# Kernel tuning notes

Hardware: AMD Instinct MI355X
Metric: run time of the kernel (lower is better)

The kernel has to match this reference:

```python
import jax, jax.numpy as jnp
import numpy as np

B, K, Z = 16384, 4096, 64  # batch, codebook size, code dim


def _linear_params(key, fan_in, fan_out):
    kw, kb = jax.random.split(key)
    lim = 1.0 / np.sqrt(fan_in)
    W = jax.random.uniform(kw, (fan_out, fan_in), jnp.float32, -lim, lim)
    b = jax.random.uniform(kb, (fan_out,), jnp.float32, -lim, lim)
    return W, b


def setup_inputs() -> dict:
    key = jax.random.key(0)
    ks = jax.random.split(key, 10)
    X = jax.random.normal(ks[0], (B, 784), jnp.float32)
    We1, be1 = _linear_params(ks[1], 784, 1000)
    We2, be2 = _linear_params(ks[2], 1000, 500)
    We3, be3 = _linear_params(ks[3], 500, 300)
    We4, be4 = _linear_params(ks[4], 300, Z)
    emb = jax.random.normal(ks[5], (K, Z), jnp.float32)  # nn.Embedding default N(0,1)
    Wd1, bd1 = _linear_params(ks[6], Z, 300)
    Wd2, bd2 = _linear_params(ks[7], 300, 500)
    Wd3, bd3 = _linear_params(ks[8], 500, 1000)
    Wd4, bd4 = _linear_params(ks[9], 1000, 784)
    return dict(X=X, We1=We1, be1=be1, We2=We2, be2=be2, We3=We3, be3=be3,
                We4=We4, be4=be4, emb=emb, Wd1=Wd1, bd1=bd1, Wd2=Wd2, bd2=bd2,
                Wd3=Wd3, bd3=bd3, Wd4=Wd4, bd4=bd4)


def _lin(x, W, b):
    return x @ W.T + b


def _nearest(query, target):
    # squared euclidean distances [Q, T] via expanded form (same math, no QxTxZ blowup)
    q2 = jnp.sum(query * query, axis=1, keepdims=True)        # [Q,1]
    t2 = jnp.sum(target * target, axis=1)                      # [T]
    d = q2 - 2.0 * (query @ target.T) + t2[None, :]            # [Q,T]
    idx = jnp.argmin(d, axis=1)                                # first min, like torch .min
    return target[idx]


def reference(X, We1, be1, We2, be2, We3, be3, We4, be4, emb,
              Wd1, bd1, Wd2, bd2, Wd3, bd3, Wd4, bd4):
    x = X.reshape(-1, 784)
    h = jax.nn.relu(_lin(x, We1, be1))
    h = jax.nn.relu(_lin(h, We2, be2))
    h = jax.nn.relu(_lin(h, We3, be3))
    Z_enc = _lin(h, We4, be4)                                  # [B,Z]
    Z_emb = _nearest(Z_enc, emb)                               # [B,Z]
    d = jax.nn.leaky_relu(_lin(Z_emb, Wd1, bd1), 0.1)
    d = jax.nn.leaky_relu(_lin(d, Wd2, bd2), 0.1)
    d = jax.nn.leaky_relu(_lin(d, Wd3, bd3), 0.1)
    Z_dec = jnp.tanh(_lin(d, Wd4, bd4)).reshape(-1, 1, 28, 28)
    Z_enc_for_emb = _nearest(emb, Z_enc)                       # [K,Z]
    return (Z_dec, Z_enc, Z_dec, Z_enc_for_emb)
```

## Files before the change

### kernel.cpp

```cpp
#include <hip/hip_runtime.h>
#include <hip/hip_bf16.h>
#include <math.h>

typedef __bf16 bf16_t;
typedef __bf16 bf16x8 __attribute__((ext_vector_type(8)));
typedef __bf16 bf16x4 __attribute__((ext_vector_type(4)));
typedef float f32x4 __attribute__((ext_vector_type(4)));

__device__ __forceinline__ void gload16(const void* g, void* l)
{
    __builtin_amdgcn_global_load_lds(
        (const __attribute__((address_space(1))) void*)g,
        (__attribute__((address_space(3))) void*)l, 16, 0, 0);
}

template<int ACT, int RB>
__global__ __launch_bounds__(256)
void np_gemm(const float* __restrict__ A, const float* __restrict__ W,
             const float* __restrict__ bias, float* __restrict__ C,
             int N, int K)
{
    constexpr int LDA = RB * 64 + 4;
    constexpr int LDB = 128 + 4;
    __shared__ __align__(16) float sA[16][LDA];
    __shared__ __align__(16) float sB[16][LDB];
    const int tid  = threadIdx.x;
    const int tx   = tid & 15, ty = tid >> 4;
    const int bRow = blockIdx.y * (RB * 64), bCol = blockIdx.x * 128;

    float4 acc[RB][2][4];
#pragma unroll
    for (int ib = 0; ib < RB; ++ib)
#pragma unroll
        for (int jb = 0; jb < 2; ++jb)
#pragma unroll
            for (int i = 0; i < 4; ++i)
                acc[ib][jb][i] = make_float4(0.f, 0.f, 0.f, 0.f);

    for (int k0 = 0; k0 < K; k0 += 16) {
        __syncthreads();
#pragma unroll
        for (int i = 0; i < RB; ++i) {
            int c  = tid + i * 256;
            int r  = c >> 2;
            int kc = (c & 3) << 2;
            int gk = k0 + kc;
            float4 av = make_float4(0.f, 0.f, 0.f, 0.f);
            if (gk < K) av = *(const float4*)(A + (size_t)(bRow + r) * K + gk);
            sA[kc + 0][r] = av.x; sA[kc + 1][r] = av.y;
            sA[kc + 2][r] = av.z; sA[kc + 3][r] = av.w;
        }
#pragma unroll
        for (int i = 0; i < 2; ++i) {
            int c  = tid + i * 256;
            int r  = c >> 2;
            int kc = (c & 3) << 2;
            int gk = k0 + kc;
            int gr = bCol + r;
            float4 bv = make_float4(0.f, 0.f, 0.f, 0.f);
            if (gr < N && gk < K) bv = *(const float4*)(W + (size_t)gr * K + gk);
            sB[kc + 0][r] = bv.x; sB[kc + 1][r] = bv.y;
            sB[kc + 2][r] = bv.z; sB[kc + 3][r] = bv.w;
        }
        __syncthreads();

#pragma unroll
        for (int kk = 0; kk < 16; ++kk) {
            float4 a[RB], b[2];
#pragma unroll
            for (int ib = 0; ib < RB; ++ib)
                a[ib] = *(const float4*)&sA[kk][ib * 64 + ty * 4];
            b[0] = *(const float4*)&sB[kk][tx * 4];
            b[1] = *(const float4*)&sB[kk][64 + tx * 4];
#pragma unroll
            for (int ib = 0; ib < RB; ++ib) {
                float ai[4] = {a[ib].x, a[ib].y, a[ib].z, a[ib].w};
#pragma unroll
                for (int i = 0; i < 4; ++i)
#pragma unroll
                    for (int jb = 0; jb < 2; ++jb) {
                        acc[ib][jb][i].x = __fmaf_rn(ai[i], b[jb].x, acc[ib][jb][i].x);
                        acc[ib][jb][i].y = __fmaf_rn(ai[i], b[jb].y, acc[ib][jb][i].y);
                        acc[ib][jb][i].z = __fmaf_rn(ai[i], b[jb].z, acc[ib][jb][i].z);
                        acc[ib][jb][i].w = __fmaf_rn(ai[i], b[jb].w, acc[ib][jb][i].w);
                    }
            }
        }
    }

#pragma unroll
    for (int jb = 0; jb < 2; ++jb) {
        int col = bCol + jb * 64 + tx * 4;
        if (col >= N) continue;
        float4 bb = *(const float4*)(bias + col);
#pragma unroll
        for (int ib = 0; ib < RB; ++ib)
#pragma unroll
            for (int i = 0; i < 4; ++i) {
                int row = bRow + ib * 64 + ty * 4 + i;
                float4 v = acc[ib][jb][i];
                float4 o;
                o.x = __fadd_rn(v.x, bb.x); o.y = __fadd_rn(v.y, bb.y);
                o.z = __fadd_rn(v.z, bb.z); o.w = __fadd_rn(v.w, bb.w);
                if (ACT == 1) {
                    o.x = o.x > 0.f ? o.x : 0.f; o.y = o.y > 0.f ? o.y : 0.f;
                    o.z = o.z > 0.f ? o.z : 0.f; o.w = o.w > 0.f ? o.w : 0.f;
                }
                *(float4*)(C + (size_t)row * N + col) = o;
            }
    }
}

__global__ void k_split(const float* __restrict__ src, bf16_t* __restrict__ hi,
                        bf16_t* __restrict__ lo, int rows, int K, int rowsP, int Kp)
{
    int e = blockIdx.x * 256 + threadIdx.x;
    if (e >= rowsP * Kp) return;
    int r = e / Kp, k = e - r * Kp;
    float v = (r < rows && k < K) ? src[(size_t)r * K + k] : 0.f;
    bf16_t h = (bf16_t)v;
    bf16_t l = (bf16_t)(v - (float)h);
    hi[e] = h; lo[e] = l;
}

template<int ACT, int OUT>
__global__ __launch_bounds__(256)
void gemm_planes(const bf16_t* __restrict__ Ahi, const bf16_t* __restrict__ Alo,
                 const bf16_t* __restrict__ Bhi, const bf16_t* __restrict__ Blo,
                 const float* __restrict__ bias,
                 float* __restrict__ C0, float* __restrict__ C1,
                 bf16_t* __restrict__ Phi, bf16_t* __restrict__ Plo,
                 int N, int Kp, int Kpn)
{
    __shared__ __align__(16) bf16_t sA[2][128][32];
    __shared__ __align__(16) bf16_t sB[2][128][32];

    const int tid  = threadIdx.x;
    const int bRow = blockIdx.y * 128;
    const int bCol = blockIdx.x * 128;
    const int wave = tid >> 6;
    const int lane = tid & 63;
    const int wr   = (wave >> 1) * 64;
    const int wc   = (wave & 1) * 64;
    const int quad = lane >> 4;
    const int l15  = lane & 15;

    f32x4 acc[4][4];
#pragma unroll
    for (int i = 0; i < 4; ++i)
#pragma unroll
        for (int j = 0; j < 4; ++j) acc[i][j] = (f32x4){0.f, 0.f, 0.f, 0.f};

    for (int k0 = 0; k0 < Kp; k0 += 32) {
        __syncthreads();
#pragma unroll
        for (int i = 0; i < 2; ++i) {
            int c    = tid + i * 256;
            int row  = c >> 2;
            int koff = (c & 3) << 3;
            size_t ga = (size_t)(bRow + row) * Kp + (k0 + koff);
            size_t gb = (size_t)(bCol + row) * Kp + (k0 + koff);
            gload16(Ahi + ga, &sA[0][row][koff]);
            gload16(Alo + ga, &sA[1][row][koff]);
            gload16(Bhi + gb, &sB[0][row][koff]);
            gload16(Blo + gb, &sB[1][row][koff]);
        }
        __syncthreads();

        bf16x8 af[2][4], bfr[2][4];
#pragma unroll
        for (int t = 0; t < 2; ++t)
#pragma unroll
            for (int i = 0; i < 4; ++i) {
                af[t][i]  = *(const bf16x8*)&sA[t][wr + i * 16 + l15][quad * 8];
                bfr[t][i] = *(const bf16x8*)&sB[t][wc + i * 16 + l15][quad * 8];
            }
#pragma unroll
        for (int i = 0; i < 4; ++i)
#pragma unroll
            for (int j = 0; j < 4; ++j)
#pragma unroll
                for (int ta = 0; ta < 2; ++ta)
#pragma unroll
                    for (int tb = 0; tb < 2 - ta; ++tb)
                        acc[i][j] = __builtin_amdgcn_mfma_f32_16x16x32_bf16(
                            af[ta][i], bfr[tb][j], acc[i][j], 0, 0, 0);
    }

#pragma unroll
    for (int j = 0; j < 4; ++j) {
        int col = bCol + wc + j * 16 + l15;
        if (OUT == 0) {
            if (col >= N) continue;
            float bv = bias[col];
#pragma unroll
            for (int i = 0; i < 4; ++i)
#pragma unroll
                for (int r = 0; r < 4; ++r) {
                    int row = bRow + wr + i * 16 + quad * 4 + r;
                    float v = acc[i][j][r] + bv;
                    if (ACT == 1)      v = v > 0.f ? v : 0.f;
                    else if (ACT == 2) v = v >= 0.f ? v : 0.1f * v;
                    else if (ACT == 3) v = tanhf(v);
                    size_t o = (size_t)row * N + col;
                    C0[o] = v;
                    if (C1) C1[o] = v;
                }
        } else {
            if (col >= Kpn) continue;
            const bool real = col < N;
            float bv = real ? bias[col] : 0.f;
#pragma unroll
            for (int i = 0; i < 4; ++i)
#pragma unroll
                for (int r = 0; r < 4; ++r) {
                    int row = bRow + wr + i * 16 + quad * 4 + r;
                    float v = 0.f;
                    if (real) {
                        v = acc[i][j][r] + bv;
                        if (ACT == 1)      v = v > 0.f ? v : 0.f;
                        else if (ACT == 2) v = v >= 0.f ? v : 0.1f * v;
                        else if (ACT == 3) v = tanhf(v);
                    }
                    bf16_t h = (bf16_t)v;
                    bf16_t l = (bf16_t)(v - (float)h);
                    size_t o = (size_t)row * Kpn + col;
                    Phi[o] = h; Plo[o] = l;
                }
        }
    }
}

__global__ __launch_bounds__(256)
void k_nearest(const float* __restrict__ Q, const float* __restrict__ C,
               const float* __restrict__ q2a, const float* __restrict__ cn2,
               int chunk, float* __restrict__ pd, int* __restrict__ pi)
{
    __shared__ __align__(16) float sc[64][64];
    __shared__ __align__(16) float sn[64];
    const int tid = threadIdx.x;
    const int q   = blockIdx.x * 256 + tid;
    const int G   = gridDim.y;

    float qr[64];
    const float4* qp = (const float4*)(Q + (size_t)q * 64);
#pragma unroll
    for (int i = 0; i < 16; ++i) ((float4*)qr)[i] = qp[i];
    const float q2 = q2a[q];

    float best = 3.4e38f;
    int   bi   = 0x7fffffff;
    const int c0 = blockIdx.y * chunk;

    for (int cb = 0; cb < chunk; cb += 64) {
        __syncthreads();
        const float4* gp = (const float4*)(C + (size_t)(c0 + cb) * 64);
#pragma unroll
        for (int i = 0; i < 4; ++i) {
            int e = tid + i * 256;
            ((float4*)&sc[0][0])[e] = gp[e];
        }
        if (tid < 64) sn[tid] = cn2[c0 + cb + tid];
        __syncthreads();

        for (int c = 0; c < 64; c += 4) {
            float a0 = 0.f, a1 = 0.f, a2 = 0.f, a3 = 0.f;
            const float4* e0 = (const float4*)&sc[c + 0][0];
            const float4* e1 = (const float4*)&sc[c + 1][0];
            const float4* e2p = (const float4*)&sc[c + 2][0];
            const float4* e3 = (const float4*)&sc[c + 3][0];
#pragma unroll
            for (int z = 0; z < 16; ++z) {
                float4 q4 = ((float4*)qr)[z];
                float4 v0 = e0[z], v1 = e1[z], v2 = e2p[z], v3 = e3[z];
                a0 = __fmaf_rn(q4.x, v0.x, a0); a0 = __fmaf_rn(q4.y, v0.y, a0);
                a0 = __fmaf_rn(q4.z, v0.z, a0); a0 = __fmaf_rn(q4.w, v0.w, a0);
                a1 = __fmaf_rn(q4.x, v1.x, a1); a1 = __fmaf_rn(q4.y, v1.y, a1);
                a1 = __fmaf_rn(q4.z, v1.z, a1); a1 = __fmaf_rn(q4.w, v1.w, a1);
                a2 = __fmaf_rn(q4.x, v2.x, a2); a2 = __fmaf_rn(q4.y, v2.y, a2);
                a2 = __fmaf_rn(q4.z, v2.z, a2); a2 = __fmaf_rn(q4.w, v2.w, a2);
                a3 = __fmaf_rn(q4.x, v3.x, a3); a3 = __fmaf_rn(q4.y, v3.y, a3);
                a3 = __fmaf_rn(q4.z, v3.z, a3); a3 = __fmaf_rn(q4.w, v3.w, a3);
            }
            float d;
            d = __fadd_rn(__fsub_rn(q2, __fmul_rn(2.f, a0)), sn[c + 0]);
            if (d < best) { best = d; bi = c0 + cb + c + 0; }
            d = __fadd_rn(__fsub_rn(q2, __fmul_rn(2.f, a1)), sn[c + 1]);
            if (d < best) { best = d; bi = c0 + cb + c + 1; }
            d = __fadd_rn(__fsub_rn(q2, __fmul_rn(2.f, a2)), sn[c + 2]);
            if (d < best) { best = d; bi = c0 + cb + c + 2; }
            d = __fadd_rn(__fsub_rn(q2, __fmul_rn(2.f, a3)), sn[c + 3]);
            if (d < best) { best = d; bi = c0 + cb + c + 3; }
        }
    }
    pd[(size_t)q * G + blockIdx.y] = best;
    pi[(size_t)q * G + blockIdx.y] = bi;
}

__global__ void k_reduce(const float* __restrict__ pd, const int* __restrict__ pi,
                         int G, int NQ, int* __restrict__ out)
{
    int q = blockIdx.x * blockDim.x + threadIdx.x;
    if (q >= NQ) return;
    float best = 3.4e38f; int bi = 0;
    for (int g = 0; g < G; ++g) {
        float d = pd[(size_t)q * G + g];
        if (d < best) { best = d; bi = pi[(size_t)q * G + g]; }
    }
    out[q] = bi;
}

__global__ void k_gather(const float* __restrict__ src, const int* __restrict__ idx,
                         float* __restrict__ dst, int nsrc)
{
    int r = blockIdx.x, z = threadIdx.x;
    int i = idx[r];
    i = i < 0 ? 0 : (i >= nsrc ? nsrc - 1 : i);
    dst[(size_t)r * 64 + z] = src[(size_t)i * 64 + z];
}

__global__ void k_gather_split(const float* __restrict__ src, const int* __restrict__ idx,
                               bf16_t* __restrict__ hi, bf16_t* __restrict__ lo, int nsrc)
{
    int r = blockIdx.x, z = threadIdx.x;
    int i = idx[r];
    i = i < 0 ? 0 : (i >= nsrc ? nsrc - 1 : i);
    float v = src[(size_t)i * 64 + z];
    bf16_t h = (bf16_t)v;
    bf16_t l = (bf16_t)(v - (float)h);
    hi[(size_t)r * 64 + z] = h;
    lo[(size_t)r * 64 + z] = l;
}

__global__ void k_norm2(const float* __restrict__ s, float* __restrict__ o, int rows)
{
    int r0 = blockIdx.x * blockDim.x + threadIdx.x;
    if (r0 >= rows) return;
    const float* p = s + (size_t)r0 * 64;
    float r[8];
#pragma unroll
    for (int j = 0; j < 8; ++j) r[j] = __fmul_rn(p[j], p[j]);
#pragma unroll
    for (int i = 8; i < 64; i += 8)
#pragma unroll
        for (int j = 0; j < 8; ++j)
            r[j] = __fadd_rn(r[j], __fmul_rn(p[i + j], p[i + j]));
    float t01 = __fadd_rn(r[0], r[1]), t23 = __fadd_rn(r[2], r[3]);
    float t45 = __fadd_rn(r[4], r[5]), t67 = __fadd_rn(r[6], r[7]);
    o[r0] = __fadd_rn(__fadd_rn(t01, t23), __fadd_rn(t45, t67));
}

extern "C" void kernel_launch(void* const* d_in, const int* in_sizes, int n_in,
                              void* d_out, int out_size, void* d_ws, size_t ws_size,
                              hipStream_t stream)
{
    const int B  = 16384;
    const int KC = 4096;

    const float* X   = (const float*)d_in[0];
    const float* We1 = (const float*)d_in[1];
    const float* be1 = (const float*)d_in[2];
    const float* We2 = (const float*)d_in[3];
    const float* be2 = (const float*)d_in[4];
    const float* We3 = (const float*)d_in[5];
    const float* be3 = (const float*)d_in[6];
    const float* We4 = (const float*)d_in[7];
    const float* be4 = (const float*)d_in[8];
    const float* emb = (const float*)d_in[9];
    const float* Wd1 = (const float*)d_in[10];
    const float* bd1 = (const float*)d_in[11];
    const float* Wd2 = (const float*)d_in[12];
    const float* bd2 = (const float*)d_in[13];
    const float* Wd3 = (const float*)d_in[14];
    const float* bd3 = (const float*)d_in[15];
    const float* Wd4 = (const float*)d_in[16];
    const float* bd4 = (const float*)d_in[17];

    float* out = (float*)d_out;
    const size_t OFF1 = (size_t)B * 784;
    const size_t OFF2 = OFF1 + (size_t)B * 64;
    const size_t OFF3 = OFF2 + (size_t)B * 784;
    float* zenc = out + OFF1;

    const size_t FIXED = (size_t)16 << 20;
    int MQ;
    if      (ws_size >= FIXED + (size_t)16384 * 7424) MQ = 16384;
    else if (ws_size >= FIXED + (size_t)8192  * 7424) MQ = 8192;
    else                                              MQ = 4096;
    const int NQn = B / MQ;

    char* ws = (char*)d_ws;
    size_t off = 0;
    auto alloc = [&](size_t bytes) -> void* {
        void* p = ws + off;
        off = (off + bytes + 255) & ~(size_t)255;
        return p;
    };
    float* pd    = (float*)alloc((size_t)262144 * 4);
    int*   pi    = (int*)alloc((size_t)262144 * 4);
    int*   idx1  = (int*)alloc((size_t)B * 4);
    int*   idx2  = (int*)alloc((size_t)KC * 4);
    float* e2    = (float*)alloc((size_t)KC * 4);
    float* z2    = (float*)alloc((size_t)B * 4);
    bf16_t* zembh = (bf16_t*)alloc((size_t)B * 64 * 2);
    bf16_t* zembl = (bf16_t*)alloc((size_t)B * 64 * 2);
    bf16_t* wp1h = (bf16_t*)alloc((size_t)384 * 64 * 2);
    bf16_t* wp1l = (bf16_t*)alloc((size_t)384 * 64 * 2);
    bf16_t* wp2h = (bf16_t*)alloc((size_t)512 * 320 * 2);
    bf16_t* wp2l = (bf16_t*)alloc((size_t)512 * 320 * 2);
    bf16_t* wp3h = (bf16_t*)alloc((size_t)1024 * 512 * 2);
    bf16_t* wp3l = (bf16_t*)alloc((size_t)1024 * 512 * 2);
    bf16_t* wp4h = (bf16_t*)alloc((size_t)896 * 1024 * 2);
    bf16_t* wp4l = (bf16_t*)alloc((size_t)896 * 1024 * 2);
    char* big = (char*)alloc((size_t)MQ * 7424);
    float* h1 = (float*)big;
    float* h2 = (float*)(big + (size_t)MQ * 4000);
    float* h3 = (float*)(big + (size_t)MQ * 6000);
    bf16_t* d1h = (bf16_t*)big;
    bf16_t* d1l = (bf16_t*)(big + (size_t)MQ * 640);
    bf16_t* d2h = (bf16_t*)(big + (size_t)MQ * 1280);
    bf16_t* d2l = (bf16_t*)(big + (size_t)MQ * 2304);
    bf16_t* d3h = (bf16_t*)(big + (size_t)MQ * 3328);
    bf16_t* d3l = (bf16_t*)(big + (size_t)MQ * 5376);

    dim3 blk(256);
    const dim3 eg1(8, MQ / 128), eg2(4, MQ / 64), eg3(3, MQ / 64), eg4(1, MQ / 64);
    const dim3 dq1(3, MQ / 128), dq2(4, MQ / 128), dq3(8, MQ / 128), dq4(7, MQ / 128);

    k_split<<<dim3((384 * 64    + 255) / 256), blk, 0, stream>>>(Wd1, wp1h, wp1l, 300, 64, 384, 64);
    k_split<<<dim3((512 * 320   + 255) / 256), blk, 0, stream>>>(Wd2, wp2h, wp2l, 500, 300, 512, 320);
    k_split<<<dim3((1024 * 512  + 255) / 256), blk, 0, stream>>>(Wd3, wp3h, wp3l, 1000, 500, 1024, 512);
    k_split<<<dim3((896 * 1024  + 255) / 256), blk, 0, stream>>>(Wd4, wp4h, wp4l, 784, 1000, 896, 1024);

    for (int q = 0; q < NQn; ++q) {
        const float* Xq = X + (size_t)q * MQ * 784;
        np_gemm<1, 2><<<eg1, blk, 0, stream>>>(Xq, We1, be1, h1, 1000, 784);
        np_gemm<1, 1><<<eg2, blk, 0, stream>>>(h1, We2, be2, h2, 500, 1000);
        np_gemm<1, 1><<<eg3, blk, 0, stream>>>(h2, We3, be3, h3, 300, 500);
        np_gemm<0, 1><<<eg4, blk, 0, stream>>>(h3, We4, be4,
                                               zenc + (size_t)q * MQ * 64, 64, 300);
    }

    k_norm2<<<dim3((KC + 255) / 256), blk, 0, stream>>>(emb, e2, KC);
    k_norm2<<<dim3((B + 255) / 256),  blk, 0, stream>>>(zenc, z2, B);

    k_nearest<<<dim3(64, 16), blk, 0, stream>>>(zenc, emb, z2, e2, 256, pd, pi);
    k_reduce <<<dim3(B / 256), blk, 0, stream>>>(pd, pi, 16, B, idx1);
    k_gather_split<<<dim3(B), dim3(64), 0, stream>>>(emb, idx1, zembh, zembl, KC);

    k_nearest<<<dim3(16, 64), blk, 0, stream>>>(emb, zenc, e2, z2, 256, pd, pi);
    k_reduce <<<dim3(KC / 256), blk, 0, stream>>>(pd, pi, 64, KC, idx2);
    k_gather <<<dim3(KC), dim3(64), 0, stream>>>(zenc, idx2, out + OFF3, B);

    for (int q = 0; q < NQn; ++q) {
        gemm_planes<2, 1><<<dq1, blk, 0, stream>>>(
            zembh + (size_t)q * MQ * 64, zembl + (size_t)q * MQ * 64,
            wp1h, wp1l, bd1, nullptr, nullptr, d1h, d1l, 300, 64, 320);
        gemm_planes<2, 1><<<dq2, blk, 0, stream>>>(
            d1h, d1l, wp2h, wp2l, bd2, nullptr, nullptr, d2h, d2l, 500, 320, 512);
        gemm_planes<2, 1><<<dq3, blk, 0, stream>>>(
            d2h, d2l, wp3h, wp3l, bd3, nullptr, nullptr, d3h, d3l, 1000, 512, 1024);
        gemm_planes<3, 0><<<dq4, blk, 0, stream>>>(
            d3h, d3l, wp4h, wp4l, bd4,
            out + (size_t)q * MQ * 784, out + OFF2 + (size_t)q * MQ * 784,
            nullptr, nullptr, 784, 1024, 0);
    }

    (void)in_sizes; (void)n_in; (void)out_size;
}
```

Before: 1.424 ms.

## Rewrite encoder FP32 GEMMs with padded weights, async LDS loads and swizzled tiles

Replaces the encoder's scalar-store FP32 GEMM with a new kernel. It loads 32-wide K tiles straight into LDS using global_load_lds, in an XOR-swizzled row-major layout, and all layers now use 128-row block tiles. Encoder weights are first copied into zero-padded buffers so inner K loops need no bounds checks, and intermediate activations use padded strides. The aim is to cut LDS transpose stores, register staging and global load overhead, at the cost of extra padding kernels, more workspace and a changed summation order.

Result: no change. 1.445 ms (+1.5%).

```diff
diff --git a/kernel.cpp b/kernel.cpp
--- a/kernel.cpp
+++ b/kernel.cpp
@@ -14,101 +14,120 @@
         (__attribute__((address_space(3))) void*)l, 16, 0, 0);
 }
 
-template<int ACT, int RB>
+template<int ACT, int CB>
 __global__ __launch_bounds__(256)
-void np_gemm(const float* __restrict__ A, const float* __restrict__ W,
-             const float* __restrict__ bias, float* __restrict__ C,
-             int N, int K)
-{
-    constexpr int LDA = RB * 64 + 4;
-    constexpr int LDB = 128 + 4;
-    __shared__ __align__(16) float sA[16][LDA];
-    __shared__ __align__(16) float sB[16][LDB];
-    const int tid  = threadIdx.x;
-    const int tx   = tid & 15, ty = tid >> 4;
-    const int bRow = blockIdx.y * (RB * 64), bCol = blockIdx.x * 128;
-
-    float4 acc[RB][2][4];
-#pragma unroll
-    for (int ib = 0; ib < RB; ++ib)
-#pragma unroll
-        for (int jb = 0; jb < 2; ++jb)
-#pragma unroll
-            for (int i = 0; i < 4; ++i)
-                acc[ib][jb][i] = make_float4(0.f, 0.f, 0.f, 0.f);
-
-    for (int k0 = 0; k0 < K; k0 += 16) {
-        __syncthreads();
-#pragma unroll
-        for (int i = 0; i < RB; ++i) {
-            int c  = tid + i * 256;
-            int r  = c >> 2;
-            int kc = (c & 3) << 2;
-            int gk = k0 + kc;
-            float4 av = make_float4(0.f, 0.f, 0.f, 0.f);
-            if (gk < K) av = *(const float4*)(A + (size_t)(bRow + r) * K + gk);
-            sA[kc + 0][r] = av.x; sA[kc + 1][r] = av.y;
-            sA[kc + 2][r] = av.z; sA[kc + 3][r] = av.w;
-        }
-#pragma unroll
-        for (int i = 0; i < 2; ++i) {
-            int c  = tid + i * 256;
-            int r  = c >> 2;
-            int kc = (c & 3) << 2;
-            int gk = k0 + kc;
-            int gr = bCol + r;
-            float4 bv = make_float4(0.f, 0.f, 0.f, 0.f);
-            if (gr < N && gk < K) bv = *(const float4*)(W + (size_t)gr * K + gk);
-            sB[kc + 0][r] = bv.x; sB[kc + 1][r] = bv.y;
-            sB[kc + 2][r] = bv.z; sB[kc + 3][r] = bv.w;
-        }
-        __syncthreads();
-
-#pragma unroll
-        for (int kk = 0; kk < 16; ++kk) {
-            float4 a[RB], b[2];
-#pragma unroll
-            for (int ib = 0; ib < RB; ++ib)
-                a[ib] = *(const float4*)&sA[kk][ib * 64 + ty * 4];
-            b[0] = *(const float4*)&sB[kk][tx * 4];
-            b[1] = *(const float4*)&sB[kk][64 + tx * 4];
-#pragma unroll
-            for (int ib = 0; ib < RB; ++ib) {
-                float ai[4] = {a[ib].x, a[ib].y, a[ib].z, a[ib].w};
-#pragma unroll
-                for (int i = 0; i < 4; ++i)
-#pragma unroll
-                    for (int jb = 0; jb < 2; ++jb) {
-                        acc[ib][jb][i].x = __fmaf_rn(ai[i], b[jb].x, acc[ib][jb][i].x);
-                        acc[ib][jb][i].y = __fmaf_rn(ai[i], b[jb].y, acc[ib][jb][i].y);
-                        acc[ib][jb][i].z = __fmaf_rn(ai[i], b[jb].z, acc[ib][jb][i].z);
-                        acc[ib][jb][i].w = __fmaf_rn(ai[i], b[jb].w, acc[ib][jb][i].w);
-                    }
+void np_gemm2(const float* __restrict__ A, const float* __restrict__ W,
+              const float* __restrict__ bias, float* __restrict__ C,
+              int N, int Cstride, int KP, int KA, int Kreal)
+{
+    __shared__ __align__(16) float sA[128 * 32];
+    __shared__ __align__(16) float sB[CB * 64 * 32];
+    const int tid = threadIdx.x;
+    const int tx  = tid & 15, ty = tid >> 4;
+    const int bRow = blockIdx.y * 128, bCol = blockIdx.x * (CB * 64);
+
+    float acc[8][CB * 4];
+#pragma unroll
+    for (int i = 0; i < 8; ++i)
+#pragma unroll
+        for (int j = 0; j < CB * 4; ++j) acc[i][j] = 0.f;
+
+    const int aswz = ty & 7;
+    const int bswz = tx & 7;
+
+    for (int k0 = 0; k0 < KP; k0 += 32) {
+        __syncthreads();
+        if (k0 + 32 <= Kreal) {
+#pragma unroll
+            for (int i = 0; i < 4; ++i) {
+                int L = tid + i * 256;
+                int r = L >> 3, cc = L & 7;
+                int gc = cc ^ ((r >> 2) & 7);
+                gload16(A + (size_t)(bRow + r) * KA + (k0 + gc * 4), sA + L * 4);
             }
-        }
-    }
-
-#pragma unroll
-    for (int jb = 0; jb < 2; ++jb) {
-        int col = bCol + jb * 64 + tx * 4;
-        if (col >= N) continue;
-        float4 bb = *(const float4*)(bias + col);
-#pragma unroll
-        for (int ib = 0; ib < RB; ++ib)
+        } else {
+#pragma unroll
+            for (int i = 0; i < 4; ++i) {
+                int L = tid + i * 256;
+                int r = L >> 3, cc = L & 7;
+                int gc = cc ^ ((r >> 2) & 7);
+                int gk = k0 + gc * 4;
+                float4 v = make_float4(0.f, 0.f, 0.f, 0.f);
+                if (gk < Kreal) v = *(const float4*)(A + (size_t)(bRow + r) * KA + gk);
+                *(float4*)(sA + L * 4) = v;
+            }
+        }
+#pragma unroll
+        for (int i = 0; i < CB * 2; ++i) {
+            int L = tid + i * 256;
+            int r = L >> 3, cc = L & 7;
+            int gc = cc ^ ((r >> 2) & 7);
+            gload16(W + (size_t)(bCol + r) * KP + (k0 + gc * 4), sB + L * 4);
+        }
+        __syncthreads();
+
+#pragma unroll
+        for (int kc = 0; kc < 8; ++kc) {
+            const int ac = ((kc ^ aswz) << 2);
+            const int bc = ((kc ^ bswz) << 2);
+            float4 b4[CB][4];
+#pragma unroll
+            for (int jb = 0; jb < CB; ++jb)
+#pragma unroll
+                for (int j = 0; j < 4; ++j)
+                    b4[jb][j] = *(const float4*)(sB + (jb * 64 + tx * 4 + j) * 32 + bc);
+#pragma unroll
+            for (int ib = 0; ib < 2; ++ib)
+#pragma unroll
+                for (int i = 0; i < 4; ++i) {
+                    float4 a4 = *(const float4*)(sA + (ib * 64 + ty * 4 + i) * 32 + ac);
+#pragma unroll
+                    for (int jb = 0; jb < CB; ++jb)
+#pragma unroll
+                        for (int j = 0; j < 4; ++j) {
+                            float& o = acc[ib * 4 + i][jb * 4 + j];
+                            o = __fmaf_rn(a4.x, b4[jb][j].x, o);
+                            o = __fmaf_rn(a4.y, b4[jb][j].y, o);
+                            o = __fmaf_rn(a4.z, b4[jb][j].z, o);
+                            o = __fmaf_rn(a4.w, b4[jb][j].w, o);
+                        }
+                }
+        }
+    }
+
+#pragma unroll
+    for (int jb = 0; jb < CB; ++jb) {
+        int col4 = bCol + jb * 64 + tx * 4;
+        if (col4 >= Cstride) continue;
+#pragma unroll
+        for (int ib = 0; ib < 2; ++ib)
 #pragma unroll
             for (int i = 0; i < 4; ++i) {
                 int row = bRow + ib * 64 + ty * 4 + i;
-                float4 v = acc[ib][jb][i];
-                float4 o;
-                o.x = __fadd_rn(v.x, bb.x); o.y = __fadd_rn(v.y, bb.y);
-                o.z = __fadd_rn(v.z, bb.z); o.w = __fadd_rn(v.w, bb.w);
-                if (ACT == 1) {
-                    o.x = o.x > 0.f ? o.x : 0.f; o.y = o.y > 0.f ? o.y : 0.f;
-                    o.z = o.z > 0.f ? o.z : 0.f; o.w = o.w > 0.f ? o.w : 0.f;
+                float ov[4];
+#pragma unroll
+                for (int j = 0; j < 4; ++j) {
+                    int col = col4 + j;
+                    float v = 0.f;
+                    if (col < N) {
+                        v = __fadd_rn(acc[ib * 4 + i][jb * 4 + j], bias[col]);
+                        if (ACT == 1) v = v > 0.f ? v : 0.f;
+                    }
+                    ov[j] = v;
                 }
-                *(float4*)(C + (size_t)row * N + col) = o;
+                *(float4*)(C + (size_t)row * Cstride + col4) =
+                    make_float4(ov[0], ov[1], ov[2], ov[3]);
             }
     }
+}
+
+__global__ void k_padw(const float* __restrict__ src, float* __restrict__ dst,
+                       int rows, int K, int rowsP, int Kp)
+{
+    int e = blockIdx.x * 256 + threadIdx.x;
+    if (e >= rowsP * Kp) return;
+    int r = e / Kp, k = e - r * Kp;
+    dst[e] = (r < rows && k < K) ? src[(size_t)r * K + k] : 0.f;
 }
 
 __global__ void k_split(const float* __restrict__ src, bf16_t* __restrict__ hi,
@@ -382,7 +401,7 @@
     const size_t OFF3 = OFF2 + (size_t)B * 784;
     float* zenc = out + OFF1;
 
-    const size_t FIXED = (size_t)16 << 20;
+    const size_t FIXED = (size_t)24 << 20;
     int MQ;
     if      (ws_size >= FIXED + (size_t)16384 * 7424) MQ = 16384;
     else if (ws_size >= FIXED + (size_t)8192  * 7424) MQ = 8192;
@@ -402,6 +421,10 @@
     int*   idx2  = (int*)alloc((size_t)KC * 4);
     float* e2    = (float*)alloc((size_t)KC * 4);
     float* z2    = (float*)alloc((size_t)B * 4);
+    float* we1p = (float*)alloc((size_t)1024 * 800 * 4);
+    float* we2p = (float*)alloc((size_t)512 * 1024 * 4);
+    float* we3p = (float*)alloc((size_t)384 * 512 * 4);
+    float* we4p = (float*)alloc((size_t)128 * 320 * 4);
     bf16_t* zembh = (bf16_t*)alloc((size_t)B * 64 * 2);
     bf16_t* zembl = (bf16_t*)alloc((size_t)B * 64 * 2);
     bf16_t* wp1h = (bf16_t*)alloc((size_t)384 * 64 * 2);
@@ -414,8 +437,8 @@
     bf16_t* wp4l = (bf16_t*)alloc((size_t)896 * 1024 * 2);
     char* big = (char*)alloc((size_t)MQ * 7424);
     float* h1 = (float*)big;
-    float* h2 = (float*)(big + (size_t)MQ * 4000);
-    float* h3 = (float*)(big + (size_t)MQ * 6000);
+    float* h2 = (float*)(big + (size_t)MQ * 4096);
+    float* h3 = (float*)(big + (size_t)MQ * 6144);
     bf16_t* d1h = (bf16_t*)big;
     bf16_t* d1l = (bf16_t*)(big + (size_t)MQ * 640);
     bf16_t* d2h = (bf16_t*)(big + (size_t)MQ * 1280);
@@ -424,21 +447,25 @@
     bf16_t* d3l = (bf16_t*)(big + (size_t)MQ * 5376);
 
     dim3 blk(256);
-    const dim3 eg1(8, MQ / 128), eg2(4, MQ / 64), eg3(3, MQ / 64), eg4(1, MQ / 64);
+    const dim3 eg1(8, MQ / 128), eg2(8, MQ / 128), eg3(6, MQ / 128), eg4(2, MQ / 128);
     const dim3 dq1(3, MQ / 128), dq2(4, MQ / 128), dq3(8, MQ / 128), dq4(7, MQ / 128);
 
-    k_split<<<dim3((384 * 64    + 255) / 256), blk, 0, stream>>>(Wd1, wp1h, wp1l, 300, 64, 384, 64);
-    k_split<<<dim3((512 * 320   + 255) / 256), blk, 0, stream>>>(Wd2, wp2h, wp2l, 500, 300, 512, 320);
-    k_split<<<dim3((1024 * 512  + 255) / 256), blk, 0, stream>>>(Wd3, wp3h, wp3l, 1000, 500, 1024, 512);
-    k_split<<<dim3((896 * 1024  + 255) / 256), blk, 0, stream>>>(Wd4, wp4h, wp4l, 784, 1000, 896, 1024);
+    k_padw<<<dim3((1024 * 800 + 255) / 256), blk, 0, stream>>>(We1, we1p, 1000, 784, 1024, 800);
+    k_padw<<<dim3((512 * 1024 + 255) / 256), blk, 0, stream>>>(We2, we2p, 500, 1000, 512, 1024);
+    k_padw<<<dim3((384 * 512  + 255) / 256), blk, 0, stream>>>(We3, we3p, 300, 500, 384, 512);
+    k_padw<<<dim3((128 * 320  + 255) / 256), blk, 0, stream>>>(We4, we4p, 64, 300, 128, 320);
+    k_split<<<dim3((384 * 64   + 255) / 256), blk, 0, stream>>>(Wd1, wp1h, wp1l, 300, 64, 384, 64);
+    k_split<<<dim3((512 * 320  + 255) / 256), blk, 0, stream>>>(Wd2, wp2h, wp2l, 500, 300, 512, 320);
+    k_split<<<dim3((1024 * 512 + 255) / 256), blk, 0, stream>>>(Wd3, wp3h, wp3l, 1000, 500, 1024, 512);
+    k_split<<<dim3((896 * 1024 + 255) / 256), blk, 0, stream>>>(Wd4, wp4h, wp4l, 784, 1000, 896, 1024);
 
     for (int q = 0; q < NQn; ++q) {
         const float* Xq = X + (size_t)q * MQ * 784;
-        np_gemm<1, 2><<<eg1, blk, 0, stream>>>(Xq, We1, be1, h1, 1000, 784);
-        np_gemm<1, 1><<<eg2, blk, 0, stream>>>(h1, We2, be2, h2, 500, 1000);
-        np_gemm<1, 1><<<eg3, blk, 0, stream>>>(h2, We3, be3, h3, 300, 500);
-        np_gemm<0, 1><<<eg4, blk, 0, stream>>>(h3, We4, be4,
-                                               zenc + (size_t)q * MQ * 64, 64, 300);
+        np_gemm2<1, 2><<<eg1, blk, 0, stream>>>(Xq, we1p, be1, h1, 1000, 1024, 800, 784, 784);
+        np_gemm2<1, 1><<<eg2, blk, 0, stream>>>(h1, we2p, be2, h2, 500, 512, 1024, 1024, 1024);
+        np_gemm2<1, 1><<<eg3, blk, 0, stream>>>(h2, we3p, be3, h3, 300, 320, 512, 512, 512);
+        np_gemm2<0, 1><<<eg4, blk, 0, stream>>>(h3, we4p, be4,
+                                                zenc + (size_t)q * MQ * 64, 64, 64, 320, 320, 320);
     }
 
     k_norm2<<<dim3((KC + 255) / 256), blk, 0, stream>>>(emb, e2, KC);
```
